# Kernel tuning notes

Hardware: AMD Instinct MI355X
Metric: run time of the kernel (lower is better)

Reference implementation:

```python
import jax, jax.numpy as jnp
import numpy as np

# Mamba hyperparams (mamba_ssm defaults for d_model=128)
D_MODEL = 128
DEPTH = 8
D_INNER = 256   # expand=2
D_STATE = 16
D_CONV = 4
DT_RANK = 8     # ceil(D_MODEL/16)
EPS = 1e-5


def setup_inputs() -> dict:
    key = jax.random.key(0)
    ks = jax.random.split(key, 8)
    B, H, W = 1, 48, 48
    s = lambda k, shape, sc=0.02: jax.random.normal(k, shape, jnp.float32) * sc
    return {
        "x": jax.random.normal(ks[0], (B, D_MODEL, H, W), jnp.float32),
        "W_in": s(ks[1], (DEPTH, D_MODEL, 2 * D_INNER)),
        "conv_w": s(ks[2], (DEPTH, D_INNER, D_CONV), 0.2),
        "conv_b": jnp.zeros((DEPTH, D_INNER), jnp.float32),
        "W_xproj": s(ks[3], (DEPTH, D_INNER, DT_RANK + 2 * D_STATE)),
        "W_dt": s(ks[4], (DEPTH, DT_RANK, D_INNER), 0.1),
        "b_dt": jnp.full((DEPTH, D_INNER), -4.6, jnp.float32),  # softplus ~= 0.01
        "A_log": jnp.broadcast_to(
            jnp.log(jnp.arange(1, D_STATE + 1, dtype=jnp.float32)),
            (DEPTH, D_INNER, D_STATE)).copy(),
        "D_skip": jnp.ones((DEPTH, D_INNER), jnp.float32),
        "W_out": s(ks[5], (DEPTH, D_INNER, D_MODEL)),
        "rms_w": jnp.ones((DEPTH, D_MODEL), jnp.float32),
    }


def _rmsnorm(x, w):
    return x * jax.lax.rsqrt(jnp.mean(x * x, axis=-1, keepdims=True) + EPS) * w


def _mamba_layer(x, Wi, cw, cb, Wx, Wdt, bdt, Alog, Dp, Wo):
    # x: [B, L, D_MODEL]
    B, L, _ = x.shape
    xz = x @ Wi                                   # [B, L, 2*d_inner]
    xi, z = jnp.split(xz, 2, axis=-1)
    # causal depthwise conv1d, kernel D_CONV
    xp = jnp.pad(xi, ((0, 0), (D_CONV - 1, 0), (0, 0)))
    xc = sum(xp[:, k:k + L, :] * cw[:, k] for k in range(D_CONV)) + cb
    xc = jax.nn.silu(xc)                          # [B, L, d_inner]
    dbl = xc @ Wx                                 # [B, L, dt_rank + 2*d_state]
    dt_r = dbl[..., :DT_RANK]
    Bs = dbl[..., DT_RANK:DT_RANK + D_STATE]      # [B, L, d_state]
    Cs = dbl[..., DT_RANK + D_STATE:]
    dt = jax.nn.softplus(dt_r @ Wdt + bdt)        # [B, L, d_inner]
    A = -jnp.exp(Alog)                            # [d_inner, d_state]
    dA = jnp.exp(dt[..., None] * A)               # [B, L, d_inner, d_state]
    dBx = (dt * xc)[..., None] * Bs[:, :, None, :]
    # linear recurrence h_t = dA_t * h_{t-1} + dBx_t via parallel scan
    def comb(l, r):
        al, bl = l
        ar, br = r
        return ar * al, ar * bl + br
    _, h = jax.lax.associative_scan(comb, (dA, dBx), axis=1)
    y = jnp.einsum('blds,bls->bld', h, Cs) + Dp * xc
    y = y * jax.nn.silu(z)
    return y @ Wo                                 # [B, L, D_MODEL]


def reference(x, W_in, conv_w, conv_b, W_xproj, W_dt, b_dt, A_log, D_skip, W_out, rms_w):
    B, C, H, W = x.shape
    seq = x.reshape(B, C, H * W).transpose(0, 2, 1)  # [B, L, C]
    for l in range(DEPTH):
        seq = _mamba_layer(seq, W_in[l], conv_w[l], conv_b[l], W_xproj[l],
                           W_dt[l], b_dt[l], A_log[l], D_skip[l], W_out[l])
        seq = _rmsnorm(seq, rms_w[l])
    return seq.reshape(B, H, W, C).transpose(0, 3, 1, 2)
```

## Files before the change

### kernel.cpp

```cpp
#include <hip/hip_runtime.h>
#include <math.h>

#define LSEQ 2304
#define DM 128
#define DI 256
#define DS 16
#define RK 8
#define NCH 576
#define CLEN 4
#define NG 24
#define GS 24
#define NSI (DI*DS)
#define EPSF 1e-5f

__device__ __forceinline__ float silu_f(float s) { return s / (1.f + __expf(-s)); }
__device__ __forceinline__ float softplus_f(float x) { return (x > 20.f) ? x : log1pf(__expf(x)); }

template<bool FIRST>
__global__ __launch_bounds__(256, 4)
void k_in(const float* __restrict__ seq, const float* __restrict__ x0,
          const float* __restrict__ Wi,
          const float* __restrict__ cw, const float* __restrict__ cbias,
          float* __restrict__ xc_g, float* __restrict__ sz_g) {
    __shared__ float As[11 * 128];
    const int l0 = blockIdx.x * 8;
    const int half = blockIdx.y & 1;
    const bool isZ = blockIdx.y >= 2;
    const int tid = threadIdx.x;

    for (int idx = tid; idx < 11 * 128; idx += 256) {
        const int r = idx >> 7, cc = idx & 127;
        const int l = l0 - 3 + r;
        As[idx] = (l >= 0) ? (FIRST ? x0[cc * LSEQ + l] : seq[l * DM + cc]) : 0.f;
    }
    __syncthreads();

    const int c = tid & 127;
    const int rg = tid >> 7;
    const int d = half * 128 + c;

    if (!isZ) {
        float ax[7] = {0.f, 0.f, 0.f, 0.f, 0.f, 0.f, 0.f};
        for (int k4 = 0; k4 < 32; ++k4) {
            float bv[4];
#pragma unroll
            for (int u = 0; u < 4; ++u) bv[u] = Wi[(k4 * 4 + u) * 512 + d];
#pragma unroll
            for (int r = 0; r < 7; ++r) {
                const float4 a4 = *(const float4*)&As[(rg * 4 + r) * 128 + k4 * 4];
                ax[r] += a4.x * bv[0] + a4.y * bv[1] + a4.z * bv[2] + a4.w * bv[3];
            }
        }
        const float w0 = cw[d * 4 + 0], w1 = cw[d * 4 + 1];
        const float w2 = cw[d * 4 + 2], w3 = cw[d * 4 + 3];
        const float cbv = cbias[d];
#pragma unroll
        for (int rr = 0; rr < 4; ++rr) {
            const float v = silu_f(cbv + w0 * ax[rr] + w1 * ax[rr + 1] +
                                   w2 * ax[rr + 2] + w3 * ax[rr + 3]);
            xc_g[(l0 + rg * 4 + rr) * DI + d] = v;
        }
    } else {
        float az[4] = {0.f, 0.f, 0.f, 0.f};
        for (int k4 = 0; k4 < 32; ++k4) {
            float bv[4];
#pragma unroll
            for (int u = 0; u < 4; ++u) bv[u] = Wi[(k4 * 4 + u) * 512 + 256 + d];
#pragma unroll
            for (int r = 0; r < 4; ++r) {
                const float4 a4 = *(const float4*)&As[(rg * 4 + r + 3) * 128 + k4 * 4];
                az[r] += a4.x * bv[0] + a4.y * bv[1] + a4.z * bv[2] + a4.w * bv[3];
            }
        }
#pragma unroll
        for (int rr = 0; rr < 4; ++rr)
            sz_g[(l0 + rg * 4 + rr) * DI + d] = silu_f(az[rr]);
    }
}

__global__ __launch_bounds__(256, 4)
void k_mid2(const float* __restrict__ xc_g,
            const float* __restrict__ Wx,
            const float* __restrict__ Wdt, const float* __restrict__ bdt,
            const float* __restrict__ Alog,
            float* __restrict__ dbl_g, float* __restrict__ dt_g,
            float* __restrict__ P, float* __restrict__ S) {
    __shared__ float xcs[CLEN * 256];
    __shared__ float part[4 * 160];
    __shared__ float dtrs[CLEN * 8];
    __shared__ float dbls[CLEN * 32];
    const int c = blockIdx.x;
    const int l0 = c * CLEN;
    const int tid = threadIdx.x;
    const int d = tid;

    ((float4*)xcs)[tid] = ((const float4*)&xc_g[l0 * DI])[tid];
    __syncthreads();

    for (int task = tid; task < 640; task += 256) {
        const int kc = task / 160;
        const int o = task - kc * 160;
        const int r = o / 40, j = o - r * 40;
        const float* xr = &xcs[r * 256 + kc * 64];
        const float* wp = &Wx[(kc * 64) * 40 + j];
        float acc = 0.f;
#pragma unroll 8
        for (int k = 0; k < 64; ++k) acc += xr[k] * wp[k * 40];
        part[kc * 160 + o] = acc;
    }
    __syncthreads();
    if (tid < 160) {
        const float acc = part[tid] + part[160 + tid] + part[320 + tid] + part[480 + tid];
        const int r = tid / 40, j = tid - r * 40;
        if (j < RK) dtrs[r * 8 + j] = acc;
        else {
            dbls[r * 32 + (j - 8)] = acc;
            dbl_g[(l0 + r) * 32 + (j - 8)] = acc;
        }
    }
    __syncthreads();

    float dtv[CLEN], xcv[CLEN];
    {
        float wdt[8];
#pragma unroll
        for (int q = 0; q < 8; ++q) wdt[q] = Wdt[q * DI + d];
        const float bdv = bdt[d];
#pragma unroll
        for (int r = 0; r < CLEN; ++r) {
            float acc = bdv;
#pragma unroll
            for (int q = 0; q < 8; ++q) acc += dtrs[r * 8 + q] * wdt[q];
            dtv[r] = softplus_f(acc);
            dt_g[(l0 + r) * DI + d] = dtv[r];
            xcv[r] = xcs[r * 256 + d];
        }
    }

    float A[16], pr[16], hs[16];
#pragma unroll
    for (int v = 0; v < 4; ++v) {
        const float4 a4 = *(const float4*)&Alog[d * DS + v * 4];
        A[v * 4 + 0] = -__expf(a4.x);
        A[v * 4 + 1] = -__expf(a4.y);
        A[v * 4 + 2] = -__expf(a4.z);
        A[v * 4 + 3] = -__expf(a4.w);
    }
#pragma unroll
    for (int s = 0; s < 16; ++s) { pr[s] = 1.f; hs[s] = 0.f; }
#pragma unroll
    for (int t = 0; t < CLEN; ++t) {
        const float dtt = dtv[t];
        const float uv = dtt * xcv[t];
        const float* Brow = &dbls[t * 32];
#pragma unroll
        for (int s = 0; s < 16; ++s) {
            const float e = __expf(dtt * A[s]);
            pr[s] *= e;
            hs[s] = e * hs[s] + uv * Brow[s];
        }
    }
    const int base = c * NSI + d * DS;
#pragma unroll
    for (int v = 0; v < 4; ++v) {
        *(float4*)&P[base + v * 4] =
            make_float4(pr[v * 4], pr[v * 4 + 1], pr[v * 4 + 2], pr[v * 4 + 3]);
        *(float4*)&S[base + v * 4] =
            make_float4(hs[v * 4], hs[v * 4 + 1], hs[v * 4 + 2], hs[v * 4 + 3]);
    }
}

__global__ __launch_bounds__(256, 4)
void k_carry1(float* __restrict__ P, float* __restrict__ S,
              float* __restrict__ Pg, float* __restrict__ Sg) {
    const int g = blockIdx.x;
    const int i = blockIdx.y * 256 + threadIdx.x;
    float G = 0.f, Pp = 1.f;
    const int base = g * GS * NSI + i;
#pragma unroll 8
    for (int k = 0; k < GS; ++k) {
        const int idx = base + k * NSI;
        const float p = P[idx];
        const float s = S[idx];
        S[idx] = G;
        P[idx] = Pp;
        G = p * G + s;
        Pp *= p;
    }
    Pg[g * NSI + i] = Pp;
    Sg[g * NSI + i] = G;
}

__global__ __launch_bounds__(256, 4)
void k_carry2(const float* __restrict__ Pg, float* __restrict__ Sg) {
    const int i = blockIdx.x * 256 + threadIdx.x;
    float G = 0.f;
#pragma unroll 8
    for (int g = 0; g < NG; ++g) {
        const int idx = g * NSI + i;
        const float p = Pg[idx];
        const float s = Sg[idx];
        Sg[idx] = G;
        G = p * G + s;
    }
}

template<bool LAST>
__global__ __launch_bounds__(256, 2)
void k_tail(const float* __restrict__ dt_g, const float* __restrict__ xc_g,
            const float* __restrict__ dbl_g, const float* __restrict__ Alog,
            const float* __restrict__ Sloc, const float* __restrict__ Ppre,
            const float* __restrict__ Gc, const float* __restrict__ Dp,
            const float* __restrict__ sz_g, const float* __restrict__ Wo,
            const float* __restrict__ rmsw, float* __restrict__ seq,
            float* __restrict__ out) {
    __shared__ float dbls[CLEN * 32];
    __shared__ float Ys[CLEN * 256];
    __shared__ float partO[4 * CLEN * 128];
    __shared__ float Os[CLEN * 129];
    __shared__ float red[CLEN * 32];
    __shared__ float scaleS[CLEN];
    const int c = blockIdx.x;
    const int g = c / GS;
    const int l0 = c * CLEN;
    const int tid = threadIdx.x;
    const int d = tid;

    if (tid < CLEN * 32) dbls[tid] = dbl_g[l0 * 32 + tid];

    float A[16], h[16];
#pragma unroll
    for (int v = 0; v < 4; ++v) {
        const float4 a4 = *(const float4*)&Alog[d * DS + v * 4];
        A[v * 4 + 0] = -__expf(a4.x);
        A[v * 4 + 1] = -__expf(a4.y);
        A[v * 4 + 2] = -__expf(a4.z);
        A[v * 4 + 3] = -__expf(a4.w);
        const float4 s4 = *(const float4*)&Sloc[c * NSI + d * DS + v * 4];
        const float4 p4 = *(const float4*)&Ppre[c * NSI + d * DS + v * 4];
        const float4 g4 = *(const float4*)&Gc[g * NSI + d * DS + v * 4];
        h[v * 4 + 0] = s4.x + p4.x * g4.x;
        h[v * 4 + 1] = s4.y + p4.y * g4.y;
        h[v * 4 + 2] = s4.z + p4.z * g4.z;
        h[v * 4 + 3] = s4.w + p4.w * g4.w;
    }
    float dtv[CLEN], xcv[CLEN], szv[CLEN];
#pragma unroll
    for (int r = 0; r < CLEN; ++r) {
        dtv[r] = dt_g[(l0 + r) * DI + d];
        xcv[r] = xc_g[(l0 + r) * DI + d];
        szv[r] = sz_g[(l0 + r) * DI + d];
    }
    const float dskip = Dp[d];
    __syncthreads();
#pragma unroll
    for (int t = 0; t < CLEN; ++t) {
        const float dtt = dtv[t];
        const float uv = dtt * xcv[t];
        float sum = 0.f;
#pragma unroll
        for (int s = 0; s < 16; ++s) {
            const float e = __expf(dtt * A[s]);
            h[s] = e * h[s] + uv * dbls[t * 32 + s];
            sum += h[s] * dbls[t * 32 + 16 + s];
        }
        Ys[t * 256 + d] = (sum + dskip * xcv[t]) * szv[t];
    }
    __syncthreads();

    {
        const int ccp = tid & 63;
        const int kg = tid >> 6;
        float acc[CLEN][2];
#pragma unroll
        for (int r = 0; r < CLEN; ++r) { acc[r][0] = 0.f; acc[r][1] = 0.f; }
        const float* wp = &Wo[(kg * 64) * DM + ccp * 2];
        const float* yp = &Ys[kg * 64];
#pragma unroll 8
        for (int k = 0; k < 64; ++k) {
            const float2 w2 = *(const float2*)(wp + k * DM);
#pragma unroll
            for (int r = 0; r < CLEN; ++r) {
                const float yv = yp[r * 256 + k];
                acc[r][0] += yv * w2.x;
                acc[r][1] += yv * w2.y;
            }
        }
#pragma unroll
        for (int r = 0; r < CLEN; ++r) {
            partO[(kg * CLEN + r) * 128 + ccp * 2 + 0] = acc[r][0];
            partO[(kg * CLEN + r) * 128 + ccp * 2 + 1] = acc[r][1];
        }
        __syncthreads();
        for (int idx = tid; idx < CLEN * 128; idx += 256) {
            const int r = idx >> 7, cc = idx & 127;
            Os[r * 129 + cc] = partO[(0 * CLEN + r) * 128 + cc] +
                               partO[(1 * CLEN + r) * 128 + cc] +
                               partO[(2 * CLEN + r) * 128 + cc] +
                               partO[(3 * CLEN + r) * 128 + cc];
        }
        __syncthreads();
    }

    if (tid < CLEN * 32) {
        const int r = tid >> 5, part = tid & 31;
        float ss = 0.f;
#pragma unroll
        for (int i = 0; i < 4; ++i) {
            const float v = Os[r * 129 + part * 4 + i];
            ss += v * v;
        }
        red[tid] = ss;
    }
    __syncthreads();
    if (tid < CLEN) {
        float ss = 0.f;
#pragma unroll
        for (int p = 0; p < 32; ++p) ss += red[tid * 32 + p];
        scaleS[tid] = rsqrtf(ss * (1.f / DM) + EPSF);
    }
    __syncthreads();
    if (LAST) {
        for (int idx = tid; idx < CLEN * DM; idx += 256) {
            const int r = idx >> 7, cc = idx & 127;
            out[cc * LSEQ + (l0 + r)] = Os[r * 129 + cc] * scaleS[r] * rmsw[cc];
        }
    } else {
        for (int idx = tid; idx < CLEN * DM; idx += 256) {
            const int r = idx >> 7, cc = idx & 127;
            seq[(l0 + r) * DM + cc] = Os[r * 129 + cc] * scaleS[r] * rmsw[cc];
        }
    }
}

extern "C" void kernel_launch(void* const* d_in, const int* in_sizes, int n_in,
                              void* d_out, int out_size, void* d_ws, size_t ws_size,
                              hipStream_t stream) {
    const float* x    = (const float*)d_in[0];
    const float* W_in = (const float*)d_in[1];
    const float* cw   = (const float*)d_in[2];
    const float* cb   = (const float*)d_in[3];
    const float* Wx   = (const float*)d_in[4];
    const float* Wdt  = (const float*)d_in[5];
    const float* bdt  = (const float*)d_in[6];
    const float* Alog = (const float*)d_in[7];
    const float* Dp   = (const float*)d_in[8];
    const float* Wo   = (const float*)d_in[9];
    const float* rmsw = (const float*)d_in[10];
    float* out = (float*)d_out;

    float* ws   = (float*)d_ws;
    float* seq  = ws; ws += LSEQ * DM;
    float* szb  = ws; ws += LSEQ * DI;
    float* xcb  = ws; ws += LSEQ * DI;
    float* dtb  = ws; ws += LSEQ * DI;
    float* dblb = ws; ws += LSEQ * 32;
    float* Pb   = ws; ws += NCH * NSI;
    float* Sb   = ws; ws += NCH * NSI;
    float* Pgb  = ws; ws += NG * NSI;
    float* Sgb  = ws; ws += NG * NSI;

    for (int layer = 0; layer < 8; ++layer) {
        const float* Wi_l   = W_in + (size_t)layer * DM * 512;
        const float* cw_l   = cw   + (size_t)layer * DI * 4;
        const float* cb_l   = cb   + (size_t)layer * DI;
        const float* Wx_l   = Wx   + (size_t)layer * DI * 40;
        const float* Wdt_l  = Wdt  + (size_t)layer * RK * DI;
        const float* bdt_l  = bdt  + (size_t)layer * DI;
        const float* Alog_l = Alog + (size_t)layer * DI * DS;
        const float* Dp_l   = Dp   + (size_t)layer * DI;
        const float* Wo_l   = Wo   + (size_t)layer * DI * DM;
        const float* rmsw_l = rmsw + (size_t)layer * DM;

        if (layer == 0)
            k_in<true><<<dim3(288, 4), 256, 0, stream>>>(seq, x, Wi_l, cw_l, cb_l,
                                                         xcb, szb);
        else
            k_in<false><<<dim3(288, 4), 256, 0, stream>>>(seq, x, Wi_l, cw_l, cb_l,
                                                          xcb, szb);

        k_mid2<<<NCH, 256, 0, stream>>>(xcb, Wx_l, Wdt_l, bdt_l, Alog_l,
                                        dblb, dtb, Pb, Sb);

        k_carry1<<<dim3(NG, 16), 256, 0, stream>>>(Pb, Sb, Pgb, Sgb);
        k_carry2<<<16, 256, 0, stream>>>(Pgb, Sgb);

        if (layer == 7)
            k_tail<true><<<NCH, 256, 0, stream>>>(dtb, xcb, dblb, Alog_l, Sb, Pb,
                                                  Sgb, Dp_l, szb, Wo_l, rmsw_l,
                                                  seq, out);
        else
            k_tail<false><<<NCH, 256, 0, stream>>>(dtb, xcb, dblb, Alog_l, Sb, Pb,
                                                   Sgb, Dp_l, szb, Wo_l, rmsw_l,
                                                   seq, out);
    }
}
```

Before: 559.9 us.

## Fold group-carry scan into tail kernel, dropping separate carry2 launch

Removes the k_carry2 kernel, which scanned group-level products and sums serially across 24 groups. Each tail block now redoes the prefix over the preceding groups for its own state slice directly from Pg/Sg, so one launch per layer disappears. The cost is redundant work: later chunks read up to 23 groups of carry data. Tail launch bounds also go from 2 to 3 blocks per SM, trading registers for occupancy.

```diff
diff --git a/kernel.cpp b/kernel.cpp
--- a/kernel.cpp
+++ b/kernel.cpp
@@ -191,26 +191,13 @@
     Sg[g * NSI + i] = G;
 }
 
-__global__ __launch_bounds__(256, 4)
-void k_carry2(const float* __restrict__ Pg, float* __restrict__ Sg) {
-    const int i = blockIdx.x * 256 + threadIdx.x;
-    float G = 0.f;
-#pragma unroll 8
-    for (int g = 0; g < NG; ++g) {
-        const int idx = g * NSI + i;
-        const float p = Pg[idx];
-        const float s = Sg[idx];
-        Sg[idx] = G;
-        G = p * G + s;
-    }
-}
-
 template<bool LAST>
-__global__ __launch_bounds__(256, 2)
+__global__ __launch_bounds__(256, 3)
 void k_tail(const float* __restrict__ dt_g, const float* __restrict__ xc_g,
             const float* __restrict__ dbl_g, const float* __restrict__ Alog,
             const float* __restrict__ Sloc, const float* __restrict__ Ppre,
-            const float* __restrict__ Gc, const float* __restrict__ Dp,
+            const float* __restrict__ Pg, const float* __restrict__ Sg,
+            const float* __restrict__ Dp,
             const float* __restrict__ sz_g, const float* __restrict__ Wo,
             const float* __restrict__ rmsw, float* __restrict__ seq,
             float* __restrict__ out) {
@@ -228,6 +215,22 @@
 
     if (tid < CLEN * 32) dbls[tid] = dbl_g[l0 * 32 + tid];
 
+    float G[16];
+#pragma unroll
+    for (int s = 0; s < 16; ++s) G[s] = 0.f;
+    for (int gg = 0; gg < g; ++gg) {
+        const int gb = gg * NSI + d * DS;
+#pragma unroll
+        for (int v = 0; v < 4; ++v) {
+            const float4 p4 = *(const float4*)&Pg[gb + v * 4];
+            const float4 s4 = *(const float4*)&Sg[gb + v * 4];
+            G[v * 4 + 0] = p4.x * G[v * 4 + 0] + s4.x;
+            G[v * 4 + 1] = p4.y * G[v * 4 + 1] + s4.y;
+            G[v * 4 + 2] = p4.z * G[v * 4 + 2] + s4.z;
+            G[v * 4 + 3] = p4.w * G[v * 4 + 3] + s4.w;
+        }
+    }
+
     float A[16], h[16];
 #pragma unroll
     for (int v = 0; v < 4; ++v) {
@@ -238,11 +241,10 @@
         A[v * 4 + 3] = -__expf(a4.w);
         const float4 s4 = *(const float4*)&Sloc[c * NSI + d * DS + v * 4];
         const float4 p4 = *(const float4*)&Ppre[c * NSI + d * DS + v * 4];
-        const float4 g4 = *(const float4*)&Gc[g * NSI + d * DS + v * 4];
-        h[v * 4 + 0] = s4.x + p4.x * g4.x;
-        h[v * 4 + 1] = s4.y + p4.y * g4.y;
-        h[v * 4 + 2] = s4.z + p4.z * g4.z;
-        h[v * 4 + 3] = s4.w + p4.w * g4.w;
+        h[v * 4 + 0] = s4.x + p4.x * G[v * 4 + 0];
+        h[v * 4 + 1] = s4.y + p4.y * G[v * 4 + 1];
+        h[v * 4 + 2] = s4.z + p4.z * G[v * 4 + 2];
+        h[v * 4 + 3] = s4.w + p4.w * G[v * 4 + 3];
     }
     float dtv[CLEN], xcv[CLEN], szv[CLEN];
 #pragma unroll
@@ -383,15 +385,14 @@
                                         dblb, dtb, Pb, Sb);
 
         k_carry1<<<dim3(NG, 16), 256, 0, stream>>>(Pb, Sb, Pgb, Sgb);
-        k_carry2<<<16, 256, 0, stream>>>(Pgb, Sgb);
 
         if (layer == 7)
             k_tail<true><<<NCH, 256, 0, stream>>>(dtb, xcb, dblb, Alog_l, Sb, Pb,
-                                                  Sgb, Dp_l, szb, Wo_l, rmsw_l,
-                                                  seq, out);
+                                                  Pgb, Sgb, Dp_l, szb, Wo_l,
+                                                  rmsw_l, seq, out);
         else
             k_tail<false><<<NCH, 256, 0, stream>>>(dtb, xcb, dblb, Alog_l, Sb, Pb,
-                                                   Sgb, Dp_l, szb, Wo_l, rmsw_l,
-                                                   seq, out);
-    }
-}
+                                                   Pgb, Sgb, Dp_l, szb, Wo_l,
+                                                   rmsw_l, seq, out);
+    }
+}
```

New measurement: 649.6 us. +16.0%, slower.
